# Kernel optimization log

Measured on AMD Instinct MI355X. Metric: run time of the kernel, lower is better.

## Reference

```python
import jax, jax.numpy as jnp
import numpy as np

N_QUBITS = 8


def _rot_mats(p):
    # p: (n, 3) -> per-qubit 2x2 unitary RX(p2) @ RZ(p1) @ RY(p0), shape (n, 2, 2)
    a, b, c = 0.5 * p[:, 0], 0.5 * p[:, 1], 0.5 * p[:, 2]
    zc = jnp.zeros_like(a).astype(jnp.complex64)
    ca, sa = jnp.cos(a), jnp.sin(a)
    ry = jnp.stack([jnp.stack([ca, -sa], -1), jnp.stack([sa, ca], -1)], -2).astype(jnp.complex64)
    eb = jnp.exp(-1j * b)
    rz = jnp.stack([jnp.stack([eb, zc], -1), jnp.stack([zc, jnp.conj(eb)], -1)], -2)
    cc = jnp.cos(c).astype(jnp.complex64)
    sc = -1j * jnp.sin(c)
    rx = jnp.stack([jnp.stack([cc, sc], -1), jnp.stack([sc, cc], -1)], -2)
    return rx @ rz @ ry


def _qgate(x, params):
    # Batched statevector simulation of the PennyLane circuit.
    # x: (B, n) RX-encoding angles; params: (depth, n, 3). Wire 0 = most-significant bit.
    B, n = x.shape
    half = 0.5 * x
    # RX(x)|0> per qubit = [cos(x/2), -i sin(x/2)]
    amps = jnp.stack([jnp.cos(half).astype(jnp.complex64), (-1j) * jnp.sin(half)], axis=-1)  # (B,n,2)
    state = amps[:, 0]  # (B, 2)
    for q in range(1, n):
        state = (state[:, :, None] * amps[:, q][:, None, :]).reshape(B, -1)
    for d in range(params.shape[0]):
        U = _rot_mats(params[d])  # (n, 2, 2)
        for w in range(n):
            s = state.reshape(B, 2 ** w, 2, -1)
            s = jnp.einsum('ab,xlbr->xlar', U[w], s)
            state = s.reshape(B, -1)
        for c in range(n - 1):  # CNOT chain (c controls c+1)
            s = state.reshape(B, 2 ** c, 2, 2, -1)
            s = jnp.stack([s[:, :, 0], s[:, :, 1, ::-1]], axis=2)
            state = s.reshape(B, -1)
    probs = state.real ** 2 + state.imag ** 2  # (B, 2**n)
    k = np.arange(2 ** n)
    signs = (1.0 - 2.0 * (((k[None, :] >> (n - 1 - np.arange(n)[:, None])) & 1))).astype(np.float32)
    return probs @ jnp.asarray(signs).T  # (B, n) Pauli-Z expvals


def _apply_gate_list(x, params_list):
    # params_list: (n_gates, depth, n, 3); gates applied sequentially
    for g in range(params_list.shape[0]):
        x = _qgate(x, params_list[g])
    return x


def setup_inputs() -> dict:
    key = jax.random.key(0)
    ks = jax.random.split(key, 10)
    T, B, D, H, P, NQ, DP = 32, 64, 512, 512, 64, N_QUBITS, 2
    inputs = jax.random.normal(ks[0], (T, B, D), jnp.float32)
    W_proj = jax.random.normal(ks[1], (P, D + H), jnp.float32) / jnp.sqrt(jnp.float32(D + H))
    b_proj = jax.random.normal(ks[2], (P,), jnp.float32) * 0.01
    W_toq = jax.random.normal(ks[3], (NQ, P), jnp.float32) / jnp.sqrt(jnp.float32(P))
    W_q2h = jax.random.normal(ks[4], (H, NQ), jnp.float32) / jnp.sqrt(jnp.float32(NQ))
    f_params = jax.random.normal(ks[5], (DP, DP, NQ, 3), jnp.float32)
    i_params = jax.random.normal(ks[6], (DP, DP, NQ, 3), jnp.float32)
    g_params = jax.random.normal(ks[7], (DP, DP, NQ, 3), jnp.float32)
    o_params = jax.random.normal(ks[8], (DP, DP, NQ, 3), jnp.float32)
    return dict(inputs=inputs, W_proj=W_proj, b_proj=b_proj, W_toq=W_toq, W_q2h=W_q2h,
                f_params=f_params, i_params=i_params, g_params=g_params, o_params=o_params)


def reference(inputs, W_proj, b_proj, W_toq, W_q2h, f_params, i_params, g_params, o_params):
    B = inputs.shape[1]
    H = W_q2h.shape[0]

    def step(carry, x):
        hx, cx = carry
        combined = jnp.concatenate([x, hx], axis=1)          # (B, D+H)
        proj = combined @ W_proj.T + b_proj                   # (B, P)
        qin = proj @ W_toq.T                                  # (B, NQ)
        f = jax.nn.sigmoid(_apply_gate_list(qin, f_params) @ W_q2h.T)
        i = jax.nn.sigmoid(_apply_gate_list(qin, i_params) @ W_q2h.T)
        g = jnp.tanh(_apply_gate_list(qin, g_params) @ W_q2h.T)
        o = jax.nn.sigmoid(_apply_gate_list(qin, o_params) @ W_q2h.T)
        cx2 = f * cx + i * g
        hx2 = o * jnp.tanh(cx2)
        return (hx2, cx2), hx2

    init = (jnp.zeros((B, H), inputs.dtype), jnp.zeros((B, H), inputs.dtype))
    (hx, cx), stacked = jax.lax.scan(step, init, inputs)
    return stacked, hx, cx
```

## Files before the change

kernel.cpp:

```cpp
#include <hip/hip_runtime.h>
#include <math.h>

#define T_STEPS 32
#define BATCH 64

#define WS_WXQ 0
#define WS_WHQ 4096
#define WS_BQ  8192
#define WS_U   8208
#define WS_XQ  9232
#define WS_AB  25616

typedef float v2f __attribute__((ext_vector_type(2)));
typedef unsigned int u32x2 __attribute__((ext_vector_type(2)));
typedef __fp16 half2v __attribute__((ext_vector_type(2)));
typedef __fp16 half4v __attribute__((ext_vector_type(4)));
typedef float f32x4 __attribute__((ext_vector_type(4)));

struct c32 { float x, y; };
__device__ __forceinline__ c32 cmul(c32 a, c32 b){ return {a.x*b.x - a.y*b.y, a.x*b.y + a.y*b.x}; }
__device__ __forceinline__ c32 cadd(c32 a, c32 b){ return {a.x+b.x, a.y+b.y}; }

__device__ __forceinline__ v2f mkv(float x, float y){ v2f r; r.x = x; r.y = y; return r; }
__device__ __forceinline__ v2f cmulv(v2f a, v2f b){
    return mkv(a.x, a.x) * b + mkv(-a.y, a.y) * mkv(b.y, b.x);
}
__device__ __forceinline__ float fast_sigmoid(float x){ return 1.f/(1.f + __expf(-x)); }
__device__ __forceinline__ float fast_tanh(float x){ float e = __expf(2.f*x); return 1.f - 2.f/(e+1.f); }

__device__ __forceinline__ half4v pk4(float a, float b, float c, float d){
#if __has_builtin(__builtin_amdgcn_cvt_pkrtz)
    half2v lo = __builtin_amdgcn_cvt_pkrtz(a, b);
    half2v hi = __builtin_amdgcn_cvt_pkrtz(c, d);
    return __builtin_shufflevector(lo, hi, 0, 1, 2, 3);
#else
    half4v r; r[0] = (__fp16)a; r[1] = (__fp16)b; r[2] = (__fp16)c; r[3] = (__fp16)d;
    return r;
#endif
}

template<int C> __device__ __forceinline__ float dppf(float v){
    return __int_as_float(__builtin_amdgcn_mov_dpp(__float_as_int(v), C, 0xF, 0xF, true));
}
__device__ __forceinline__ float swap16(float v, int lane){
#if __has_builtin(__builtin_amdgcn_permlane16_swap)
    u32x2 r = __builtin_amdgcn_permlane16_swap(__float_as_uint(v), __float_as_uint(v), false, false);
    return __uint_as_float((lane & 16) ? r.x : r.y);
#else
    return __shfl_xor(v, 16);
#endif
}
__device__ __forceinline__ float swap32(float v, int lane){
#if __has_builtin(__builtin_amdgcn_permlane32_swap)
    u32x2 r = __builtin_amdgcn_permlane32_swap(__float_as_uint(v), __float_as_uint(v), false, false);
    return __uint_as_float((lane & 32) ? r.x : r.y);
#else
    return __shfl_xor(v, 32);
#endif
}
template<int LM> __device__ __forceinline__ float lanexor(float v, int lane){
    if constexpr (LM == 1)       return dppf<0xB1>(v);
    else if constexpr (LM == 2)  return dppf<0x4E>(v);
    else if constexpr (LM == 4)  return dppf<0x1B>(dppf<0x141>(v));
    else if constexpr (LM == 8)  return dppf<0x128>(v);
    else if constexpr (LM == 16) return swap16(v, lane);
    else                         return swap32(v, lane);
}
__device__ __forceinline__ float rdl(float v, int l){
    return __int_as_float(__builtin_amdgcn_readlane(__float_as_int(v), l));
}
__device__ __forceinline__ void fsincos(float rev, float* s, float* c){
#if __has_builtin(__builtin_amdgcn_sinf) && __has_builtin(__builtin_amdgcn_cosf)
    *s = __builtin_amdgcn_sinf(rev);
    *c = __builtin_amdgcn_cosf(rev);
#else
    __sincosf(rev * 6.2831853071795864f, s, c);
#endif
}

__device__ __forceinline__ void rot_u(const float* p3, float* dst){
    float a = 0.5f * p3[0], b = 0.5f * p3[1], c = 0.5f * p3[2];
    float ca = cosf(a), sa = sinf(a);
    float cb = cosf(b), sb = sinf(b);
    float cc = cosf(c), sc = sinf(c);
    c32 eb  = {cb, -sb};
    c32 ebc = {cb,  sb};
    c32 scx = {0.f, -sc};
    c32 m00 = { eb.x * ca,  eb.y * ca};
    c32 m01 = {-eb.x * sa, -eb.y * sa};
    c32 m10 = { ebc.x * sa, ebc.y * sa};
    c32 m11 = { ebc.x * ca, ebc.y * ca};
    c32 U00 = cadd(c32{cc * m00.x, cc * m00.y}, cmul(scx, m10));
    c32 U01 = cadd(c32{cc * m01.x, cc * m01.y}, cmul(scx, m11));
    c32 U10 = cadd(cmul(scx, m00), c32{cc * m10.x, cc * m10.y});
    c32 U11 = cadd(cmul(scx, m01), c32{cc * m11.x, cc * m11.y});
    dst[0] = U00.x; dst[1] = U00.y; dst[2] = U01.x; dst[3] = U01.y;
    dst[4] = U10.x; dst[5] = U10.y; dst[6] = U11.x; dst[7] = U11.y;
}

__global__ void precompute_kernel(const float* __restrict__ W_proj,
                                  const float* __restrict__ b_proj,
                                  const float* __restrict__ W_toq,
                                  const float* __restrict__ fP, const float* __restrict__ iP,
                                  const float* __restrict__ gP, const float* __restrict__ oP,
                                  float* __restrict__ ws)
{
    int tid = threadIdx.x;
    int blk = blockIdx.x;
    if (blk < 32) {
        int idx = blk * 256 + tid;
        int q = idx >> 10, dd = idx & 1023;
        float acc = 0.f;
        for (int p = 0; p < 64; ++p) acc += W_toq[q * 64 + p] * W_proj[p * 1024 + dd];
        if (dd < 512) ws[WS_WXQ + q * 512 + dd] = acc;
        else          ws[WS_WHQ + q * 512 + (dd - 512)] = acc;
        if (idx < 8) {
            float a2 = 0.f;
            for (int p = 0; p < 64; ++p) a2 += W_toq[idx * 64 + p] * b_proj[p];
            ws[WS_BQ + idx] = a2;
        }
    } else if (blk == 32) {
        if (tid < 128) {
            int gt = tid >> 5, rest = tid & 31;
            const float* P = (gt == 0) ? fP : (gt == 1) ? iP : (gt == 2) ? gP : oP;
            int g = (rest >> 4) & 1, d = (rest >> 3) & 1, w = rest & 7;
            rot_u(P + (((g * 2 + d) * 8 + w) * 3), ws + WS_U + tid * 8);
        }
    } else {
        __shared__ float sW[8][8];
        int combo = blk - 33;
        int gt = combo >> 1, gl = combo & 1;
        if (tid < 8) {
            const float* P = (gt == 0) ? fP : (gt == 1) ? iP : (gt == 2) ? gP : oP;
            rot_u(P + (((gl * 2 + 1) * 8 + tid) * 3), &sW[tid][0]);
        }
        __syncthreads();
        int rp = tid >> 4, rr = tid & 15;
        c32 pa = {1.f, 0.f};
        #pragma unroll
        for (int w = 0; w < 4; ++w) {
            int i = (rp >> (3 - w)) & 1, j = (rr >> (3 - w)) & 1;
            c32 e = {sW[w][(i * 2 + j) * 2], sW[w][(i * 2 + j) * 2 + 1]};
            pa = cmul(pa, e);
        }
        ws[WS_AB + combo * 1024 + tid * 2]     = pa.x;
        ws[WS_AB + combo * 1024 + tid * 2 + 1] = pa.y;
        c32 pb = {1.f, 0.f};
        #pragma unroll
        for (int w = 4; w < 8; ++w) {
            int i = (rp >> (7 - w)) & 1, j = (rr >> (7 - w)) & 1;
            c32 e = {sW[w][(i * 2 + j) * 2], sW[w][(i * 2 + j) * 2 + 1]};
            pb = cmul(pb, e);
        }
        ws[WS_AB + combo * 1024 + 512 + tid * 2]     = pb.x;
        ws[WS_AB + combo * 1024 + 512 + tid * 2 + 1] = pb.y;
    }
}

__global__ void xq_kernel(const float* __restrict__ inputs, float* __restrict__ ws)
{
    __shared__ float xs[512];
    int row = blockIdx.x;
    int tid = threadIdx.x;
    xs[tid]       = inputs[row * 512 + tid];
    xs[tid + 256] = inputs[row * 512 + 256 + tid];
    __syncthreads();
    int g = tid >> 5, j = tid & 31;
    const float* w = ws + WS_WXQ + g * 512;
    float acc = 0.f;
    #pragma unroll 4
    for (int i = 0; i < 16; ++i) acc += xs[j + 32 * i] * w[j + 32 * i];
    acc += __shfl_xor(acc, 1);  acc += __shfl_xor(acc, 2);
    acc += __shfl_xor(acc, 4);  acc += __shfl_xor(acc, 8);
    acc += __shfl_xor(acc, 16);
    if (j == 0) ws[WS_XQ + row * 8 + g] = (acc + ws[WS_BQ + g]) * 0.07957747154594767f;
}

__global__ __launch_bounds__(256, 1)
void recurrence_kernel(const float* __restrict__ W_q2h,
                       const float* __restrict__ ws,
                       float* __restrict__ out)
{
    __shared__ __align__(16) float sU[1024];
    __shared__ __align__(16) float sXq[T_STEPS * 8];
    __shared__ __align__(16) float sexpW[4][8];
    __shared__ __align__(16) float qpartW[4][8];

    int tid = threadIdx.x;
    int b   = blockIdx.x;
    int wv  = tid >> 6;
    int lane = tid & 63;
    int l = lane;

    for (int i = tid; i < 1024; i += 256) sU[i] = ws[WS_U + i];
    sXq[tid] = ws[WS_XQ + ((tid >> 3) * 64 + b) * 8 + (tid & 7)];
    if (tid < 32) ((float*)qpartW)[tid] = 0.f;

    v2f wha2[4], whb2[4];
    #pragma unroll
    for (int j = 0; j < 4; ++j) {
        wha2[j] = mkv(ws[WS_WHQ + (2*j) * 512 + tid],       ws[WS_WHQ + (2*j+1) * 512 + tid]);
        whb2[j] = mkv(ws[WS_WHQ + (2*j) * 512 + tid + 256], ws[WS_WHQ + (2*j+1) * 512 + tid + 256]);
    }
    v2f w2hp[8];
    {
        float4 a0 = *(const float4*)&W_q2h[tid * 8];
        float4 a1 = *(const float4*)&W_q2h[tid * 8 + 4];
        float4 b0 = *(const float4*)&W_q2h[(tid + 256) * 8];
        float4 b1 = *(const float4*)&W_q2h[(tid + 256) * 8 + 4];
        w2hp[0] = mkv(a0.x, b0.x); w2hp[1] = mkv(a0.y, b0.y);
        w2hp[2] = mkv(a0.z, b0.z); w2hp[3] = mkv(a0.w, b0.w);
        w2hp[4] = mkv(a1.x, b1.x); w2hp[5] = mkv(a1.y, b1.y);
        w2hp[6] = mkv(a1.z, b1.z); w2hp[7] = mkv(a1.w, b1.w);
    }

    half4v ArT[2], AiT[2], nAiT[2], Brf[2], Bif[2], nBif[2];
    {
        int q4 = lane >> 4, n = lane & 15;
        #pragma unroll
        for (int gl = 0; gl < 2; ++gl) {
            const float* Ab = ws + WS_AB + (wv * 2 + gl) * 1024;
            const float* Bb = Ab + 512;
            #pragma unroll
            for (int j = 0; j < 4; ++j) {
                int k = 4 * q4 + j;
                float ar = Ab[(n * 16 + k) * 2], ai = Ab[(n * 16 + k) * 2 + 1];
                float br = Bb[(n * 16 + k) * 2], bi = Bb[(n * 16 + k) * 2 + 1];
                ArT[gl][j]  = (__fp16)ar;  AiT[gl][j] = (__fp16)ai;  nAiT[gl][j] = (__fp16)(-ai);
                Brf[gl][j]  = (__fp16)br;  Bif[gl][j] = (__fp16)bi;  nBif[gl][j] = (__fp16)(-bi);
            }
        }
    }

    __syncthreads();

    v2f sA0[2], sB0[2], sA1[2], sB1[2], sA5[2], sB5[2], sA6[2], sB6[2], sA7[2], sB7[2];
    v2f A2a[2], B2a[2], A2b[2], B2b[2];
    v2f A3a[2], B3a[2], A3b[2], B3b[2];
    v2f A4a[2], B4a[2], A4b[2], B4b[2];
    {
        int s0 = (l >> 5) & 1;
        int s1 = ((l >> 5) ^ (l >> 4)) & 1;
        int s5 = ((l >> 3) ^ (l >> 2)) & 1;
        int s6 = ((l >> 2) ^ (l >> 1)) & 1;
        int s7 = ((l >> 1) ^ l) & 1;
        int L4 = (l >> 4) & 1;
        int L3 = (l >> 3) & 1;
        #pragma unroll
        for (int gl = 0; gl < 2; ++gl) {
            const float* d0 = sU + (wv * 32 + gl * 16) * 8;
            #define CA(q,c) mkv(d0[(q)*8 + (c)*4 + 0], d0[(q)*8 + (c)*4 + 1])
            #define CB(q,c) mkv(d0[(q)*8 + (c)*4 + 3], -d0[(q)*8 + (c)*4 + 2])
            sA0[gl] = s0 ? CA(0,1) : CA(0,0);  sB0[gl] = s0 ? CB(0,1) : CB(0,0);
            sA1[gl] = s1 ? CA(1,1) : CA(1,0);  sB1[gl] = s1 ? CB(1,1) : CB(1,0);
            sA5[gl] = s5 ? CA(5,1) : CA(5,0);  sB5[gl] = s5 ? CB(5,1) : CB(5,0);
            sA6[gl] = s6 ? CA(6,1) : CA(6,0);  sB6[gl] = s6 ? CB(6,1) : CB(6,0);
            sA7[gl] = s7 ? CA(7,1) : CA(7,0);  sB7[gl] = s7 ? CB(7,1) : CB(7,0);
            A2a[gl] = L4 ? CA(2,1) : CA(2,0);  B2a[gl] = L4 ? CB(2,1) : CB(2,0);
            A2b[gl] = L4 ? CA(2,0) : CA(2,1);  B2b[gl] = L4 ? CB(2,0) : CB(2,1);
            A3a[gl] = CA(3,0);                 B3a[gl] = CB(3,0);
            A3b[gl] = CA(3,1);                 B3b[gl] = CB(3,1);
            A4a[gl] = L3 ? CA(4,1) : CA(4,0);  B4a[gl] = L3 ? CB(4,1) : CB(4,0);
            A4b[gl] = L3 ? CA(4,0) : CA(4,1);  B4b[gl] = L3 ? CB(4,0) : CB(4,1);
            #undef CA
            #undef CB
        }
    }

    const float REVC = 0.07957747154594767f;

    half4v Bsgn; f32x4 SHsgn, SHsgnR;
    {
        int q = lane & 15;
        int g4 = lane >> 4;
        int mlo = (q < 4) ? 0 : (q == 4) ? 8 : (q == 5) ? 12 : (q == 6) ? 14 : (q == 7) ? 15 : 0;
        int mhi = (q == 0) ? 8 : (q == 1) ? 12 : (q == 2) ? 14 : 15;
        #pragma unroll
        for (int j = 0; j < 4; ++j) {
            int k = 4 * g4 + j;
            float bs = (q < 8) ? ((__builtin_popcount(k & mlo) & 1) ? -1.f : 1.f) : 0.f;
            Bsgn[j] = (__fp16)bs;
            SHsgn[j]  = (__builtin_popcount(k & mhi) & 1) ? -1.f : 1.f;
            SHsgnR[j] = SHsgn[j] * REVC;
        }
    }

    const f32x4 zacc = {0.f, 0.f, 0.f, 0.f};
    float c0 = 0.f, c1 = 0.f, h0 = 0.f, h1 = 0.f;

    for (int t = 0; t < T_STEPS; ++t) {
        float ang[8];
        {
            const v2f* qw = (const v2f*)qpartW;
            const v2f* xq2 = (const v2f*)&sXq[t * 8];
            #pragma unroll
            for (int j = 0; j < 4; ++j) {
                v2f s_ = (qw[j] + qw[4 + j]) + (qw[8 + j] + qw[12 + j]) + xq2[j];
                ang[2 * j] = s_.x; ang[2 * j + 1] = s_.y;
            }
        }

        float e[8];
        #pragma unroll
        for (int gl = 0; gl < 2; ++gl) {
            float sh[8], ch[8];
            #pragma unroll
            for (int q = 0; q < 8; ++q) fsincos(ang[q], &sh[q], &ch[q]);

            v2f u0 = ch[0] * sA0[gl] + sh[0] * sB0[gl];
            v2f u1 = ch[1] * sA1[gl] + sh[1] * sB1[gl];
            v2f u5 = ch[5] * sA5[gl] + sh[5] * sB5[gl];
            v2f u6 = ch[6] * sA6[gl] + sh[6] * sB6[gl];
            v2f u7 = ch[7] * sA7[gl] + sh[7] * sB7[gl];
            v2f u2a = ch[2] * A2a[gl] + sh[2] * B2a[gl];
            v2f u2b = ch[2] * A2b[gl] + sh[2] * B2b[gl];
            v2f u3a = ch[3] * A3a[gl] + sh[3] * B3a[gl];
            v2f u3b = ch[3] * A3b[gl] + sh[3] * B3b[gl];
            v2f u4a = ch[4] * A4a[gl] + sh[4] * B4a[gl];
            v2f u4b = ch[4] * A4b[gl] + sh[4] * B4b[gl];

            v2f hi = cmulv(u0, u1);
            v2f lo = cmulv(cmulv(u5, u6), u7);
            v2f hilo = cmulv(hi, lo);
            v2f hl_a = cmulv(hilo, u4a);
            v2f hl_b = cmulv(hilo, u4b);
            v2f u23_0 = cmulv(u2a, u3a);
            v2f u23_1 = cmulv(u2a, u3b);
            v2f u23_2 = cmulv(u2b, u3b);
            v2f u23_3 = cmulv(u2b, u3a);
            v2f a0 = cmulv(u23_0, hl_a);
            v2f a1 = cmulv(u23_1, hl_b);
            v2f a2 = cmulv(u23_2, hl_a);
            v2f a3 = cmulv(u23_3, hl_b);

            half4v Sr = pk4(a0.x, a1.x, a2.x, a3.x);
            half4v Si = pk4(a0.y, a1.y, a2.y, a3.y);

            f32x4 TrT = __builtin_amdgcn_mfma_f32_16x16x16f16(Sr, ArT[gl], zacc, 0, 0, 0);
            TrT = __builtin_amdgcn_mfma_f32_16x16x16f16(Si, nAiT[gl], TrT, 0, 0, 0);
            f32x4 TiT = __builtin_amdgcn_mfma_f32_16x16x16f16(Sr, AiT[gl], zacc, 0, 0, 0);
            TiT = __builtin_amdgcn_mfma_f32_16x16x16f16(Si, ArT[gl], TiT, 0, 0, 0);
            half4v TrH = pk4(TrT[0], TrT[1], TrT[2], TrT[3]);
            half4v TiH = pk4(TiT[0], TiT[1], TiT[2], TiT[3]);
            f32x4 Xr = __builtin_amdgcn_mfma_f32_16x16x16f16(Brf[gl], TrH, zacc, 0, 0, 0);
            Xr = __builtin_amdgcn_mfma_f32_16x16x16f16(nBif[gl], TiH, Xr, 0, 0, 0);
            f32x4 Xi = __builtin_amdgcn_mfma_f32_16x16x16f16(Brf[gl], TiH, zacc, 0, 0, 0);
            Xi = __builtin_amdgcn_mfma_f32_16x16x16f16(Bif[gl], TrH, Xi, 0, 0, 0);

            f32x4 P = Xr * Xr + Xi * Xi;
            half4v Pf = pk4(P[0], P[1], P[2], P[3]);
            f32x4 Cm = __builtin_amdgcn_mfma_f32_16x16x16f16(Pf, Bsgn, zacc, 0, 0, 0);
            f32x4 Mm = Cm * ((gl == 0) ? SHsgnR : SHsgn);
            float v = (Mm[0] + Mm[1]) + (Mm[2] + Mm[3]);
            v += swap16(v, lane);
            v += swap32(v, lane);
            e[0] = rdl(v, 0); e[1] = rdl(v, 1); e[2] = rdl(v, 2); e[3] = rdl(v, 3);
            e[4] = rdl(v, 4); e[5] = rdl(v, 5); e[6] = rdl(v, 6); e[7] = rdl(v, 7);
            if (gl == 0) {
                #pragma unroll
                for (int q = 0; q < 8; ++q) ang[q] = e[q];
            }
        }
        if (lane == 0) {
            float4 e0v; e0v.x = e[0]; e0v.y = e[1]; e0v.z = e[2]; e0v.w = e[3];
            float4 e1v; e1v.x = e[4]; e1v.y = e[5]; e1v.z = e[6]; e1v.w = e[7];
            *(float4*)&sexpW[wv][0] = e0v;
            *(float4*)&sexpW[wv][4] = e1v;
        }
        __syncthreads();

        {
            v2f pre[4];
            #pragma unroll
            for (int g = 0; g < 4; ++g) {
                float4 ea = *(const float4*)&sexpW[g][0];
                float4 eb2 = *(const float4*)&sexpW[g][4];
                v2f acc = ea.x * w2hp[0] + ea.y * w2hp[1] + ea.z * w2hp[2] + ea.w * w2hp[3]
                        + eb2.x * w2hp[4] + eb2.y * w2hp[5] + eb2.z * w2hp[6] + eb2.w * w2hp[7];
                pre[g] = acc;
            }
            float f0 = fast_sigmoid(pre[0].x), i0 = fast_sigmoid(pre[1].x);
            float g0 = fast_tanh(pre[2].x),    o0 = fast_sigmoid(pre[3].x);
            c0 = f0 * c0 + i0 * g0;  h0 = o0 * fast_tanh(c0);
            float f1 = fast_sigmoid(pre[0].y), i1 = fast_sigmoid(pre[1].y);
            float g1 = fast_tanh(pre[2].y),    o1 = fast_sigmoid(pre[3].y);
            c1 = f1 * c1 + i1 * g1;  h1 = o1 * fast_tanh(c1);
            out[(t * 64 + b) * 512 + tid]       = h0;
            out[(t * 64 + b) * 512 + tid + 256] = h1;
        }

        {
            v2f pp[4];
            #pragma unroll
            for (int j = 0; j < 4; ++j) pp[j] = wha2[j] * h0 + whb2[j] * h1;
            #pragma unroll
            for (int j = 0; j < 4; ++j) {
                pp[j] += mkv(lanexor<1>(pp[j].x, lane), lanexor<1>(pp[j].y, lane));
                pp[j] += mkv(lanexor<2>(pp[j].x, lane), lanexor<2>(pp[j].y, lane));
                pp[j] += mkv(lanexor<4>(pp[j].x, lane), lanexor<4>(pp[j].y, lane));
            }
            int sel = lane & 7;
            float y = (sel == 0) ? pp[0].x : (sel == 1) ? pp[0].y
                    : (sel == 2) ? pp[1].x : (sel == 3) ? pp[1].y
                    : (sel == 4) ? pp[2].x : (sel == 5) ? pp[2].y
                    : (sel == 6) ? pp[3].x : pp[3].y;
            y += lanexor<8>(y, lane);
            y += swap16(y, lane);
            y += swap32(y, lane);
            if (lane < 8) qpartW[wv][lane] = y * REVC;
        }
        __syncthreads();
    }

    float* hx_out = out + (size_t)T_STEPS * 64 * 512;
    float* cx_out = hx_out + 64 * 512;
    hx_out[b * 512 + tid]       = h0;
    hx_out[b * 512 + tid + 256] = h1;
    cx_out[b * 512 + tid]       = c0;
    cx_out[b * 512 + tid + 256] = c1;
}

extern "C" void kernel_launch(void* const* d_in, const int* in_sizes, int n_in,
                              void* d_out, int out_size, void* d_ws, size_t ws_size,
                              hipStream_t stream)
{
    const float* inputs = (const float*)d_in[0];
    const float* W_proj = (const float*)d_in[1];
    const float* b_proj = (const float*)d_in[2];
    const float* W_toq  = (const float*)d_in[3];
    const float* W_q2h  = (const float*)d_in[4];
    const float* fP     = (const float*)d_in[5];
    const float* iP     = (const float*)d_in[6];
    const float* gP     = (const float*)d_in[7];
    const float* oP     = (const float*)d_in[8];
    float* ws  = (float*)d_ws;
    float* out = (float*)d_out;

    precompute_kernel<<<41, 256, 0, stream>>>(W_proj, b_proj, W_toq, fP, iP, gP, oP, ws);
    xq_kernel<<<T_STEPS * BATCH, 256, 0, stream>>>(inputs, ws);
    recurrence_kernel<<<BATCH, 256, 0, stream>>>(W_q2h, ws, out);
}
```

Baseline: 141.5 us.

## Fuse input projection into recurrence kernel and use LDS atomics for hidden partials

Removes the separate xq_kernel launch. Each recurrence block now computes its own 32 timesteps of input-to-qubit projections in a prologue, using float4 loads and a shuffle reduction, and stores them in shared memory. The per-wave hidden partial sums are now accumulated with shared-memory atomicAdd into a double-buffered 8-float array, so the angle setup reads 8 values instead of summing 4 per-wave copies. This saves a kernel launch and a global round trip, but the prologue is serial within only 64 blocks and the atomics add contention.

```diff
diff --git a/kernel.cpp b/kernel.cpp
--- a/kernel.cpp
+++ b/kernel.cpp
@@ -8,7 +8,6 @@
 #define WS_WHQ 4096
 #define WS_BQ  8192
 #define WS_U   8208
-#define WS_XQ  9232
 #define WS_AB  25616
 
 typedef float v2f __attribute__((ext_vector_type(2)));
@@ -157,34 +156,16 @@
     }
 }
 
-__global__ void xq_kernel(const float* __restrict__ inputs, float* __restrict__ ws)
-{
-    __shared__ float xs[512];
-    int row = blockIdx.x;
-    int tid = threadIdx.x;
-    xs[tid]       = inputs[row * 512 + tid];
-    xs[tid + 256] = inputs[row * 512 + 256 + tid];
-    __syncthreads();
-    int g = tid >> 5, j = tid & 31;
-    const float* w = ws + WS_WXQ + g * 512;
-    float acc = 0.f;
-    #pragma unroll 4
-    for (int i = 0; i < 16; ++i) acc += xs[j + 32 * i] * w[j + 32 * i];
-    acc += __shfl_xor(acc, 1);  acc += __shfl_xor(acc, 2);
-    acc += __shfl_xor(acc, 4);  acc += __shfl_xor(acc, 8);
-    acc += __shfl_xor(acc, 16);
-    if (j == 0) ws[WS_XQ + row * 8 + g] = (acc + ws[WS_BQ + g]) * 0.07957747154594767f;
-}
-
 __global__ __launch_bounds__(256, 1)
-void recurrence_kernel(const float* __restrict__ W_q2h,
+void recurrence_kernel(const float* __restrict__ inputs,
+                       const float* __restrict__ W_q2h,
                        const float* __restrict__ ws,
                        float* __restrict__ out)
 {
     __shared__ __align__(16) float sU[1024];
     __shared__ __align__(16) float sXq[T_STEPS * 8];
     __shared__ __align__(16) float sexpW[4][8];
-    __shared__ __align__(16) float qpartW[4][8];
+    __shared__ __align__(16) float qpartS[2][8];
 
     int tid = threadIdx.x;
     int b   = blockIdx.x;
@@ -192,9 +173,29 @@
     int lane = tid & 63;
     int l = lane;
 
+    const float REVC = 0.07957747154594767f;
+
     for (int i = tid; i < 1024; i += 256) sU[i] = ws[WS_U + i];
-    sXq[tid] = ws[WS_XQ + ((tid >> 3) * 64 + b) * 8 + (tid & 7)];
-    if (tid < 32) ((float*)qpartW)[tid] = 0.f;
+    if (tid < 16) ((float*)qpartS)[tid] = 0.f;
+
+    {
+        int gq = tid >> 5, jj = tid & 31;
+        const float4* wsx = (const float4*)(ws + WS_WXQ + gq * 512 + jj * 16);
+        float4 wq0 = wsx[0], wq1 = wsx[1], wq2 = wsx[2], wq3 = wsx[3];
+        float bq = ws[WS_BQ + gq];
+        for (int t2 = 0; t2 < T_STEPS; ++t2) {
+            const float4* row = (const float4*)(inputs + (t2 * 64 + b) * 512 + jj * 16);
+            float4 x0 = row[0], x1 = row[1], x2 = row[2], x3 = row[3];
+            float acc = x0.x*wq0.x + x0.y*wq0.y + x0.z*wq0.z + x0.w*wq0.w
+                      + x1.x*wq1.x + x1.y*wq1.y + x1.z*wq1.z + x1.w*wq1.w
+                      + x2.x*wq2.x + x2.y*wq2.y + x2.z*wq2.z + x2.w*wq2.w
+                      + x3.x*wq3.x + x3.y*wq3.y + x3.z*wq3.z + x3.w*wq3.w;
+            acc += __shfl_xor(acc, 1);  acc += __shfl_xor(acc, 2);
+            acc += __shfl_xor(acc, 4);  acc += __shfl_xor(acc, 8);
+            acc += __shfl_xor(acc, 16);
+            if (jj == 0) sXq[t2 * 8 + gq] = (acc + bq) * REVC;
+        }
+    }
 
     v2f wha2[4], whb2[4];
     #pragma unroll
@@ -267,8 +268,6 @@
         }
     }
 
-    const float REVC = 0.07957747154594767f;
-
     half4v Bsgn; f32x4 SHsgn, SHsgnR;
     {
         int q = lane & 15;
@@ -288,16 +287,19 @@
     const f32x4 zacc = {0.f, 0.f, 0.f, 0.f};
     float c0 = 0.f, c1 = 0.f, h0 = 0.f, h1 = 0.f;
 
+    float4 xqa = *(const float4*)&sXq[0];
+    float4 xqb = *(const float4*)&sXq[4];
+
     for (int t = 0; t < T_STEPS; ++t) {
+        int p = t & 1;
         float ang[8];
         {
-            const v2f* qw = (const v2f*)qpartW;
-            const v2f* xq2 = (const v2f*)&sXq[t * 8];
-            #pragma unroll
-            for (int j = 0; j < 4; ++j) {
-                v2f s_ = (qw[j] + qw[4 + j]) + (qw[8 + j] + qw[12 + j]) + xq2[j];
-                ang[2 * j] = s_.x; ang[2 * j + 1] = s_.y;
-            }
+            float4 qa = *(const float4*)&qpartS[p][0];
+            float4 qb = *(const float4*)&qpartS[p][4];
+            ang[0] = qa.x + xqa.x; ang[1] = qa.y + xqa.y;
+            ang[2] = qa.z + xqa.z; ang[3] = qa.w + xqa.w;
+            ang[4] = qb.x + xqb.x; ang[5] = qb.y + xqb.y;
+            ang[6] = qb.z + xqb.z; ang[7] = qb.w + xqb.w;
         }
 
         float e[8];
@@ -368,6 +370,12 @@
             *(float4*)&sexpW[wv][4] = e1v;
         }
         __syncthreads();
+
+        if (tid < 8) qpartS[p][tid] = 0.f;
+        if (t + 1 < T_STEPS) {
+            xqa = *(const float4*)&sXq[(t + 1) * 8];
+            xqb = *(const float4*)&sXq[(t + 1) * 8 + 4];
+        }
 
         {
             v2f pre[4];
@@ -407,7 +415,7 @@
             y += lanexor<8>(y, lane);
             y += swap16(y, lane);
             y += swap32(y, lane);
-            if (lane < 8) qpartW[wv][lane] = y * REVC;
+            if (lane < 8) atomicAdd(&qpartS[p ^ 1][lane], y * REVC);
         }
         __syncthreads();
     }
@@ -437,6 +445,5 @@
     float* out = (float*)d_out;
 
     precompute_kernel<<<41, 256, 0, stream>>>(W_proj, b_proj, W_toq, fP, iP, gP, oP, ws);
-    xq_kernel<<<T_STEPS * BATCH, 256, 0, stream>>>(inputs, ws);
-    recurrence_kernel<<<BATCH, 256, 0, stream>>>(W_q2h, ws, out);
-}
+    recurrence_kernel<<<BATCH, 256, 0, stream>>>(inputs, W_q2h, ws, out);
+}
```

Measured after the change: 151.7 us. 1.07x slower.
